# Performance work log

Measured on AMD Instinct MI355X. Metric: run time of the kernel, lower is better.

The kernel has to match this reference:

```python
import jax, jax.numpy as jnp
import numpy as np

E, W, S, Q, D = 256, 20, 5, 300, 512
ALPHA = 37.0  # hardcoded weight '37' in computeProto


def setup_inputs() -> dict:
    key = jax.random.key(0)
    k1, k2 = jax.random.split(key)
    x_shot = jax.random.normal(k1, (E, W, S, D), dtype=jnp.float32)
    x_query = jax.random.normal(k2, (E, Q, D), dtype=jnp.float32)
    temp = jnp.float32(10.0)
    return {"x_shot": x_shot, "x_query": x_query, "temp": temp}


def compute_proto(x_shot, x_query):
    # x_shot: [E, W, S, D], x_query: [E, Q, D]
    n_shot = x_shot.shape[2]
    shot_sum = x_shot.sum(axis=2)                      # [E, W, D]
    shot_mean = x_shot.mean(axis=2)                    # [E, W, D]
    # pairwise euclidean distance mean-vs-query: [E, W, Q]
    diff = shot_mean[:, :, None, :] - x_query[:, None, :, :]
    dist = jnp.sqrt(jnp.sum(diff * diff, axis=-1))
    weights = jax.nn.softmax(-dist, axis=-1)           # softmax over queries
    pooled = jnp.einsum('ewq,eqd->ewd', weights, x_query)  # [E, W, D]
    proto = (shot_sum + ALPHA * pooled) / (n_shot + ALPHA)
    return proto


def l2norm(x, axis=-1, eps=1e-12):
    n = jnp.sqrt(jnp.sum(x * x, axis=axis, keepdims=True))
    return x / jnp.maximum(n, eps)


def reference(x_shot, x_query, temp):
    proto = compute_proto(x_shot, x_query)             # [E, W, D]
    proto = l2norm(proto)
    q = l2norm(x_query)
    logits = temp * jnp.einsum('eqd,ewd->eqw', q, proto)  # [E, Q, W]
    return logits
```

## Files before the change

### kernel.cpp

```cpp
#include <hip/hip_runtime.h>
#include <math.h>

#define E_ 256
#define W_ 20
#define S_ 5
#define Q_ 300
#define D_ 512
#define ALPHA_ 37.0f
#define QCH 32
#define NCH 10
#define QPAD 304

typedef __attribute__((ext_vector_type(8))) short bf16x8;
typedef __attribute__((ext_vector_type(4))) float f32x4;
typedef __attribute__((ext_vector_type(2))) unsigned int u32x2;
typedef __attribute__((ext_vector_type(4))) unsigned int u32x4;

#define OFF_SS   0
#define OFF_XQ   20480
#define OFF_BUF  53248
#define OFF_Q2   77568
#define OFF_M2   78848
#define OFF_MINV 78976
#define OFF_RED  79104
#define LDS_BYTES 79744

__device__ __forceinline__ unsigned short f2bf(float x) {
    unsigned int u = __builtin_bit_cast(unsigned int, x);
    u += 0x7fffu + ((u >> 16) & 1u);
    return (unsigned short)(u >> 16);
}
__device__ __forceinline__ float bf2f(unsigned short h) {
    unsigned int u = ((unsigned int)h) << 16;
    return __builtin_bit_cast(float, u);
}

__device__ __forceinline__ bf16x8 ldfrag(const char* base, int row, int k0) {
    const int phys = (k0 >> 3) ^ (row & 7);
    return *reinterpret_cast<const bf16x8*>(base + row * 1024 + phys * 16);
}

__device__ __forceinline__ void stage_load(const float4* xq4, int c, int qcount,
                                           int tid, float4* r) {
    const int qr = tid >> 4;
    const int i  = tid & 15;
    const int qg = c * QCH + ((qr < qcount) ? qr : 0);
    const float4* row4 = xq4 + (size_t)qg * (D_ / 4);
    #pragma unroll
    for (int j = 0; j < 4; ++j) {
        const int ch = i + 16 * j;
        r[2 * j]     = row4[2 * ch];
        r[2 * j + 1] = row4[2 * ch + 1];
    }
}

template <bool WQ2>
__device__ __forceinline__ void stage_write(const float4* r, char* s_xq, float* s_q2,
                                            int c, int qcount, int tid) {
    const int qr = tid >> 4;
    const int i  = tid & 15;
    const bool valid = qr < qcount;
    float q2 = 0.f;
    #pragma unroll
    for (int j = 0; j < 4; ++j) {
        const int ch = i + 16 * j;
        float4 a = valid ? r[2 * j]     : make_float4(0.f, 0.f, 0.f, 0.f);
        float4 b = valid ? r[2 * j + 1] : make_float4(0.f, 0.f, 0.f, 0.f);
        if (WQ2) {
            q2 += a.x * a.x + a.y * a.y + a.z * a.z + a.w * a.w
                + b.x * b.x + b.y * b.y + b.z * b.z + b.w * b.w;
        }
        u32x4 v;
        v[0] = (unsigned int)f2bf(a.x) | ((unsigned int)f2bf(a.y) << 16);
        v[1] = (unsigned int)f2bf(a.z) | ((unsigned int)f2bf(a.w) << 16);
        v[2] = (unsigned int)f2bf(b.x) | ((unsigned int)f2bf(b.y) << 16);
        v[3] = (unsigned int)f2bf(b.z) | ((unsigned int)f2bf(b.w) << 16);
        *reinterpret_cast<u32x4*>(s_xq + qr * 1024 + ((ch ^ (qr & 7)) << 4)) = v;
    }
    if (WQ2) {
        q2 += __shfl_xor(q2, 1);
        q2 += __shfl_xor(q2, 2);
        q2 += __shfl_xor(q2, 4);
        q2 += __shfl_xor(q2, 8);
        if (i == 0) s_q2[c * QCH + qr] = valid ? q2 : 0.f;
    }
}

__global__ __launch_bounds__(512, 4) void fused9(const float* __restrict__ xs,
                                                 const float* __restrict__ xq,
                                                 const float* __restrict__ temp_p,
                                                 float* __restrict__ out) {
    extern __shared__ char smem[];
    char*  s_ss   = smem + OFF_SS;
    char*  s_xq   = smem + OFF_XQ;
    float* s_buf  = (float*)(smem + OFF_BUF);
    float* s_q2   = (float*)(smem + OFF_Q2);
    float* s_m2   = (float*)(smem + OFF_M2);
    float* s_minv = (float*)(smem + OFF_MINV);
    float* s_red  = (float*)(smem + OFF_RED);

    const int e    = blockIdx.x;
    const int tid  = threadIdx.x;
    const int lane = tid & 63;
    const int wv   = tid >> 6;
    const int ln15 = lane & 15;
    const int hi   = lane >> 4;

    const float*  xse = xs + (size_t)e * (W_ * S_ * D_);
    const float*  xqe = xq + (size_t)e * (Q_ * D_);
    const float4* xq4 = (const float4*)xqe;
    const float   temp = *temp_p;

    float4 buf[8];

    stage_load(xq4, 0, QCH, tid, buf);

    #pragma unroll
    for (int it = 0; it < 5; ++it) {
        const int idx = it * 512 + tid;
        const int w   = idx >> 7;
        const int dq  = idx & 127;
        const float4* p0 = reinterpret_cast<const float4*>(xse + (w * S_) * D_ + dq * 4);
        float4 a = p0[0];
        #pragma unroll
        for (int s = 1; s < S_; ++s) {
            const float4 t = p0[s * (D_ / 4)];
            a.x += t.x; a.y += t.y; a.z += t.z; a.w += t.w;
        }
        u32x2 v;
        v[0] = (unsigned int)f2bf(a.x) | ((unsigned int)f2bf(a.y) << 16);
        v[1] = (unsigned int)f2bf(a.z) | ((unsigned int)f2bf(a.w) << 16);
        *reinterpret_cast<u32x2*>(s_ss + w * 1024 + (((dq >> 1) ^ (w & 7)) << 4) +
                                  (dq & 1) * 8) = v;
    }
    __syncthreads();

    for (int w = wv; w < W_; w += 8) {
        bf16x8 v = *reinterpret_cast<const bf16x8*>(s_ss + w * 1024 + ((lane ^ (w & 7)) << 4));
        float p = 0.f;
        #pragma unroll
        for (int j = 0; j < 8; ++j) { float f = bf2f((unsigned short)v[j]); p += f * f; }
        #pragma unroll
        for (int off = 32; off; off >>= 1) p += __shfl_xor(p, off);
        if (lane == 0) s_m2[w] = p * (1.f / (S_ * S_));
    }
    __syncthreads();

    for (int c = 0; c < NCH; ++c) {
        const int qcount = (c == NCH - 1) ? (Q_ - (NCH - 1) * QCH) : QCH;
        stage_write<true>(buf, s_xq, s_q2, c, qcount, tid);
        __syncthreads();
        if (c + 1 < NCH)
            stage_load(xq4, c + 1, (c + 2 == NCH) ? (Q_ - (NCH - 1) * QCH) : QCH, tid, buf);

        if (wv < 4) {
            const int wtile = wv >> 1, qtile = wv & 1;
            f32x4 acc = {0.f, 0.f, 0.f, 0.f};
            const int arow = wtile * 4 + ln15;
            const int brow = qtile * 16 + ln15;
            #pragma unroll
            for (int k = 0; k < 16; ++k) {
                bf16x8 a = ldfrag(s_ss, arow, k * 32 + hi * 8);
                bf16x8 b = ldfrag(s_xq, brow, k * 32 + hi * 8);
                acc = __builtin_amdgcn_mfma_f32_16x16x32_bf16(a, b, acc, 0, 0, 0);
            }
            const int qloc = qtile * 16 + ln15;
            if (qloc < qcount) {
                const int qg = c * QCH + qloc;
                const float q2v = s_q2[qg];
                #pragma unroll
                for (int r = 0; r < 4; ++r) {
                    const int w = wtile * 4 + hi * 4 + r;
                    float d2 = s_m2[w] + q2v - 0.4f * acc[r];
                    s_buf[w * QPAD + qg] = -sqrtf(fmaxf(d2, 0.f));
                }
            }
        }
        __syncthreads();
    }

    for (int w = wv; w < W_; w += 8) {
        float mx = -1e30f;
        for (int q = lane; q < Q_; q += 64) mx = fmaxf(mx, s_buf[w * QPAD + q]);
        #pragma unroll
        for (int off = 32; off; off >>= 1) mx = fmaxf(mx, __shfl_xor(mx, off));
        float sm = 0.f;
        for (int q = lane; q < Q_; q += 64) {
            float ex = __expf(s_buf[w * QPAD + q] - mx);
            s_buf[w * QPAD + q] = ex;
            sm += ex;
        }
        #pragma unroll
        for (int off = 32; off; off >>= 1) sm += __shfl_xor(sm, off);
        const float inv = 1.f / sm;
        for (int q = lane; q < Q_; q += 64) s_buf[w * QPAD + q] *= inv;
    }
    __syncthreads();

    stage_load(xq4, 0, QCH, tid, buf);

    {
        float pr[W_];
        #pragma unroll
        for (int w = 0; w < W_; ++w) pr[w] = 0.f;
        for (int q0 = 0; q0 < Q_; q0 += 4) {
            const float qv0 = xqe[(q0 + 0) * D_ + tid];
            const float qv1 = xqe[(q0 + 1) * D_ + tid];
            const float qv2 = xqe[(q0 + 2) * D_ + tid];
            const float qv3 = xqe[(q0 + 3) * D_ + tid];
            #pragma unroll
            for (int w = 0; w < W_; ++w) {
                const float4 wt = *reinterpret_cast<const float4*>(&s_buf[w * QPAD + q0]);
                pr[w] += wt.x * qv0 + wt.y * qv1 + wt.z * qv2 + wt.w * qv3;
            }
        }
        const int chb = tid >> 3;
        #pragma unroll
        for (int w = 0; w < W_; ++w) {
            unsigned short h =
                *(unsigned short*)(s_ss + w * 1024 + ((chb ^ (w & 7)) << 4) + (tid & 7) * 2);
            pr[w] = (bf2f(h) + ALPHA_ * pr[w]) * (1.f / (S_ + ALPHA_));
        }
        #pragma unroll
        for (int w = 0; w < W_; ++w) {
            float p = pr[w] * pr[w];
            #pragma unroll
            for (int off = 32; off; off >>= 1) p += __shfl_xor(p, off);
            if (lane == 0) s_red[wv * W_ + w] = p;
        }
        __syncthreads();
        if (tid < W_) {
            float p = 0.f;
            #pragma unroll
            for (int k = 0; k < 8; ++k) p += s_red[k * W_ + tid];
            s_minv[tid] = 1.f / fmaxf(sqrtf(p), 1e-12f);
        }
        __syncthreads();
        #pragma unroll
        for (int w = 0; w < W_; ++w) {
            *(unsigned short*)(s_ss + w * 1024 + ((chb ^ (w & 7)) << 4) + (tid & 7) * 2) =
                f2bf(pr[w] * s_minv[w]);
        }
        __syncthreads();
    }

    const size_t eoff = (size_t)e * (Q_ * W_);
    for (int c = 0; c < NCH; ++c) {
        const int qcount = (c == NCH - 1) ? (Q_ - (NCH - 1) * QCH) : QCH;
        stage_write<false>(buf, s_xq, s_q2, c, qcount, tid);
        __syncthreads();
        if (c + 1 < NCH)
            stage_load(xq4, c + 1, (c + 2 == NCH) ? (Q_ - (NCH - 1) * QCH) : QCH, tid, buf);

        if (wv < 4) {
            const int qtile = wv >> 1, wtile = wv & 1;
            f32x4 acc = {0.f, 0.f, 0.f, 0.f};
            const int arow = qtile * 16 + ln15;
            const int brow = wtile * 4 + ln15;
            #pragma unroll
            for (int k = 0; k < 16; ++k) {
                bf16x8 a = ldfrag(s_xq, arow, k * 32 + hi * 8);
                bf16x8 b = ldfrag(s_ss, brow, k * 32 + hi * 8);
                acc = __builtin_amdgcn_mfma_f32_16x16x32_bf16(a, b, acc, 0, 0, 0);
            }
            const int w = wtile * 4 + ln15;
            #pragma unroll
            for (int r = 0; r < 4; ++r) {
                const int qloc = qtile * 16 + hi * 4 + r;
                if (qloc < qcount) {
                    const int qg = c * QCH + qloc;
                    const float scale = temp / fmaxf(sqrtf(s_q2[qg]), 1e-12f);
                    out[eoff + qg * W_ + w] = scale * acc[r];
                }
            }
        }
        __syncthreads();
    }
}

extern "C" void kernel_launch(void* const* d_in, const int* in_sizes, int n_in,
                              void* d_out, int out_size, void* d_ws, size_t ws_size,
                              hipStream_t stream) {
    const float* xs = (const float*)d_in[0];
    const float* xq = (const float*)d_in[1];
    const float* tp = (const float*)d_in[2];
    hipFuncSetAttribute(reinterpret_cast<const void*>(fused9),
                        hipFuncAttributeMaxDynamicSharedMemorySize, LDS_BYTES);
    fused9<<<E_, 512, LDS_BYTES, stream>>>(xs, xq, tp, (float*)d_out);
}
```

Baseline: 122.3 us.

## Widen block to 12 waves with 96-query chunks and packed bf16 conversion

Result: no change. 123.6 us (+1.1%).

```diff
diff --git a/kernel.cpp b/kernel.cpp
--- a/kernel.cpp
+++ b/kernel.cpp
@@ -1,4 +1,5 @@
 #include <hip/hip_runtime.h>
+#include <hip/hip_bf16.h>
 #include <math.h>
 
 #define E_ 256
@@ -7,8 +8,8 @@
 #define Q_ 300
 #define D_ 512
 #define ALPHA_ 37.0f
-#define QCH 32
-#define NCH 10
+#define QCH 96
+#define NCH 4
 #define QPAD 304
 
 typedef __attribute__((ext_vector_type(8))) short bf16x8;
@@ -18,17 +19,24 @@
 
 #define OFF_SS   0
 #define OFF_XQ   20480
-#define OFF_BUF  53248
-#define OFF_Q2   77568
-#define OFF_M2   78848
-#define OFF_MINV 78976
-#define OFF_RED  79104
-#define LDS_BYTES 79744
+#define OFF_BUF  118784
+#define OFF_Q2   143104
+#define OFF_M2   144640
+#define OFF_MINV 144768
+#define OFF_RED  144896
+#define LDS_BYTES 145536
 
 __device__ __forceinline__ unsigned short f2bf(float x) {
-    unsigned int u = __builtin_bit_cast(unsigned int, x);
-    u += 0x7fffu + ((u >> 16) & 1u);
-    return (unsigned short)(u >> 16);
+    __hip_bfloat16 h = __float2bfloat16(x);
+    unsigned short u;
+    __builtin_memcpy(&u, &h, 2);
+    return u;
+}
+__device__ __forceinline__ unsigned int pk2(float lo, float hi) {
+    __hip_bfloat162 h2 = __float22bfloat162_rn(make_float2(lo, hi));
+    unsigned int u;
+    __builtin_memcpy(&u, &h2, 4);
+    return u;
 }
 __device__ __forceinline__ float bf2f(unsigned short h) {
     unsigned int u = ((unsigned int)h) << 16;
@@ -42,13 +50,13 @@
 
 __device__ __forceinline__ void stage_load(const float4* xq4, int c, int qcount,
                                            int tid, float4* r) {
-    const int qr = tid >> 4;
-    const int i  = tid & 15;
+    const int qr = tid >> 3;
+    const int i  = tid & 7;
     const int qg = c * QCH + ((qr < qcount) ? qr : 0);
     const float4* row4 = xq4 + (size_t)qg * (D_ / 4);
     #pragma unroll
-    for (int j = 0; j < 4; ++j) {
-        const int ch = i + 16 * j;
+    for (int j = 0; j < 8; ++j) {
+        const int ch = i + 8 * j;
         r[2 * j]     = row4[2 * ch];
         r[2 * j + 1] = row4[2 * ch + 1];
     }
@@ -57,13 +65,13 @@
 template <bool WQ2>
 __device__ __forceinline__ void stage_write(const float4* r, char* s_xq, float* s_q2,
                                             int c, int qcount, int tid) {
-    const int qr = tid >> 4;
-    const int i  = tid & 15;
+    const int qr = tid >> 3;
+    const int i  = tid & 7;
     const bool valid = qr < qcount;
     float q2 = 0.f;
     #pragma unroll
-    for (int j = 0; j < 4; ++j) {
-        const int ch = i + 16 * j;
+    for (int j = 0; j < 8; ++j) {
+        const int ch = i + 8 * j;
         float4 a = valid ? r[2 * j]     : make_float4(0.f, 0.f, 0.f, 0.f);
         float4 b = valid ? r[2 * j + 1] : make_float4(0.f, 0.f, 0.f, 0.f);
         if (WQ2) {
@@ -71,25 +79,24 @@
                 + b.x * b.x + b.y * b.y + b.z * b.z + b.w * b.w;
         }
         u32x4 v;
-        v[0] = (unsigned int)f2bf(a.x) | ((unsigned int)f2bf(a.y) << 16);
-        v[1] = (unsigned int)f2bf(a.z) | ((unsigned int)f2bf(a.w) << 16);
-        v[2] = (unsigned int)f2bf(b.x) | ((unsigned int)f2bf(b.y) << 16);
-        v[3] = (unsigned int)f2bf(b.z) | ((unsigned int)f2bf(b.w) << 16);
+        v[0] = pk2(a.x, a.y);
+        v[1] = pk2(a.z, a.w);
+        v[2] = pk2(b.x, b.y);
+        v[3] = pk2(b.z, b.w);
         *reinterpret_cast<u32x4*>(s_xq + qr * 1024 + ((ch ^ (qr & 7)) << 4)) = v;
     }
     if (WQ2) {
         q2 += __shfl_xor(q2, 1);
         q2 += __shfl_xor(q2, 2);
         q2 += __shfl_xor(q2, 4);
-        q2 += __shfl_xor(q2, 8);
         if (i == 0) s_q2[c * QCH + qr] = valid ? q2 : 0.f;
     }
 }
 
-__global__ __launch_bounds__(512, 4) void fused9(const float* __restrict__ xs,
-                                                 const float* __restrict__ xq,
-                                                 const float* __restrict__ temp_p,
-                                                 float* __restrict__ out) {
+__global__ __launch_bounds__(768, 1) void fused13(const float* __restrict__ xs,
+                                                  const float* __restrict__ xq,
+                                                  const float* __restrict__ temp_p,
+                                                  float* __restrict__ out) {
     extern __shared__ char smem[];
     char*  s_ss   = smem + OFF_SS;
     char*  s_xq   = smem + OFF_XQ;
@@ -111,31 +118,33 @@
     const float4* xq4 = (const float4*)xqe;
     const float   temp = *temp_p;
 
-    float4 buf[8];
+    float4 buf[16];
 
     stage_load(xq4, 0, QCH, tid, buf);
 
     #pragma unroll
-    for (int it = 0; it < 5; ++it) {
-        const int idx = it * 512 + tid;
-        const int w   = idx >> 7;
-        const int dq  = idx & 127;
-        const float4* p0 = reinterpret_cast<const float4*>(xse + (w * S_) * D_ + dq * 4);
-        float4 a = p0[0];
-        #pragma unroll
-        for (int s = 1; s < S_; ++s) {
-            const float4 t = p0[s * (D_ / 4)];
-            a.x += t.x; a.y += t.y; a.z += t.z; a.w += t.w;
-        }
-        u32x2 v;
-        v[0] = (unsigned int)f2bf(a.x) | ((unsigned int)f2bf(a.y) << 16);
-        v[1] = (unsigned int)f2bf(a.z) | ((unsigned int)f2bf(a.w) << 16);
-        *reinterpret_cast<u32x2*>(s_ss + w * 1024 + (((dq >> 1) ^ (w & 7)) << 4) +
-                                  (dq & 1) * 8) = v;
+    for (int it = 0; it < 4; ++it) {
+        const int idx = it * 768 + tid;
+        if (idx < W_ * 128) {
+            const int w  = idx >> 7;
+            const int dq = idx & 127;
+            const float4* p0 = reinterpret_cast<const float4*>(xse + (w * S_) * D_ + dq * 4);
+            float4 a = p0[0];
+            #pragma unroll
+            for (int s = 1; s < S_; ++s) {
+                const float4 t = p0[s * (D_ / 4)];
+                a.x += t.x; a.y += t.y; a.z += t.z; a.w += t.w;
+            }
+            u32x2 v;
+            v[0] = pk2(a.x, a.y);
+            v[1] = pk2(a.z, a.w);
+            *reinterpret_cast<u32x2*>(s_ss + w * 1024 + (((dq >> 1) ^ (w & 7)) << 4) +
+                                      (dq & 1) * 8) = v;
+        }
     }
     __syncthreads();
 
-    for (int w = wv; w < W_; w += 8) {
+    for (int w = wv; w < W_; w += 12) {
         bf16x8 v = *reinterpret_cast<const bf16x8*>(s_ss + w * 1024 + ((lane ^ (w & 7)) << 4));
         float p = 0.f;
         #pragma unroll
@@ -153,33 +162,31 @@
         if (c + 1 < NCH)
             stage_load(xq4, c + 1, (c + 2 == NCH) ? (Q_ - (NCH - 1) * QCH) : QCH, tid, buf);
 
-        if (wv < 4) {
-            const int wtile = wv >> 1, qtile = wv & 1;
-            f32x4 acc = {0.f, 0.f, 0.f, 0.f};
-            const int arow = wtile * 4 + ln15;
-            const int brow = qtile * 16 + ln15;
-            #pragma unroll
-            for (int k = 0; k < 16; ++k) {
-                bf16x8 a = ldfrag(s_ss, arow, k * 32 + hi * 8);
-                bf16x8 b = ldfrag(s_xq, brow, k * 32 + hi * 8);
-                acc = __builtin_amdgcn_mfma_f32_16x16x32_bf16(a, b, acc, 0, 0, 0);
-            }
-            const int qloc = qtile * 16 + ln15;
-            if (qloc < qcount) {
-                const int qg = c * QCH + qloc;
-                const float q2v = s_q2[qg];
-                #pragma unroll
-                for (int r = 0; r < 4; ++r) {
-                    const int w = wtile * 4 + hi * 4 + r;
-                    float d2 = s_m2[w] + q2v - 0.4f * acc[r];
-                    s_buf[w * QPAD + qg] = -sqrtf(fmaxf(d2, 0.f));
-                }
-            }
-        }
-        __syncthreads();
-    }
-
-    for (int w = wv; w < W_; w += 8) {
+        const int qtile = wv >> 1, wtile = wv & 1;
+        f32x4 acc = {0.f, 0.f, 0.f, 0.f};
+        const int arow = wtile * 4 + ln15;
+        const int brow = qtile * 16 + ln15;
+        #pragma unroll
+        for (int k = 0; k < 16; ++k) {
+            bf16x8 a = ldfrag(s_ss, arow, k * 32 + hi * 8);
+            bf16x8 b = ldfrag(s_xq, brow, k * 32 + hi * 8);
+            acc = __builtin_amdgcn_mfma_f32_16x16x32_bf16(a, b, acc, 0, 0, 0);
+        }
+        const int qloc = qtile * 16 + ln15;
+        if (qloc < qcount) {
+            const int qg = c * QCH + qloc;
+            const float q2v = s_q2[qg];
+            #pragma unroll
+            for (int r = 0; r < 4; ++r) {
+                const int w = wtile * 4 + hi * 4 + r;
+                float d2 = s_m2[w] + q2v - 0.4f * acc[r];
+                s_buf[w * QPAD + qg] = -sqrtf(fmaxf(d2, 0.f));
+            }
+        }
+        __syncthreads();
+    }
+
+    for (int w = wv; w < W_; w += 12) {
         float mx = -1e30f;
         for (int q = lane; q < Q_; q += 64) mx = fmaxf(mx, s_buf[w * QPAD + q]);
         #pragma unroll
@@ -201,32 +208,34 @@
 
     {
         float pr[W_];
-        #pragma unroll
-        for (int w = 0; w < W_; ++w) pr[w] = 0.f;
-        for (int q0 = 0; q0 < Q_; q0 += 4) {
-            const float qv0 = xqe[(q0 + 0) * D_ + tid];
-            const float qv1 = xqe[(q0 + 1) * D_ + tid];
-            const float qv2 = xqe[(q0 + 2) * D_ + tid];
-            const float qv3 = xqe[(q0 + 3) * D_ + tid];
+        if (tid < 512) {
+            #pragma unroll
+            for (int w = 0; w < W_; ++w) pr[w] = 0.f;
+            for (int q0 = 0; q0 < Q_; q0 += 4) {
+                const float qv0 = xqe[(q0 + 0) * D_ + tid];
+                const float qv1 = xqe[(q0 + 1) * D_ + tid];
+                const float qv2 = xqe[(q0 + 2) * D_ + tid];
+                const float qv3 = xqe[(q0 + 3) * D_ + tid];
+                #pragma unroll
+                for (int w = 0; w < W_; ++w) {
+                    const float4 wt = *reinterpret_cast<const float4*>(&s_buf[w * QPAD + q0]);
+                    pr[w] += wt.x * qv0 + wt.y * qv1 + wt.z * qv2 + wt.w * qv3;
+                }
+            }
+            const int chb = tid >> 3;
             #pragma unroll
             for (int w = 0; w < W_; ++w) {
-                const float4 wt = *reinterpret_cast<const float4*>(&s_buf[w * QPAD + q0]);
-                pr[w] += wt.x * qv0 + wt.y * qv1 + wt.z * qv2 + wt.w * qv3;
-            }
-        }
-        const int chb = tid >> 3;
-        #pragma unroll
-        for (int w = 0; w < W_; ++w) {
-            unsigned short h =
-                *(unsigned short*)(s_ss + w * 1024 + ((chb ^ (w & 7)) << 4) + (tid & 7) * 2);
-            pr[w] = (bf2f(h) + ALPHA_ * pr[w]) * (1.f / (S_ + ALPHA_));
-        }
-        #pragma unroll
-        for (int w = 0; w < W_; ++w) {
-            float p = pr[w] * pr[w];
-            #pragma unroll
-            for (int off = 32; off; off >>= 1) p += __shfl_xor(p, off);
-            if (lane == 0) s_red[wv * W_ + w] = p;
+                unsigned short h =
+                    *(unsigned short*)(s_ss + w * 1024 + ((chb ^ (w & 7)) << 4) + (tid & 7) * 2);
+                pr[w] = (bf2f(h) + ALPHA_ * pr[w]) * (1.f / (S_ + ALPHA_));
+            }
+            #pragma unroll
+            for (int w = 0; w < W_; ++w) {
+                float p = pr[w] * pr[w];
+                #pragma unroll
+                for (int off = 32; off; off >>= 1) p += __shfl_xor(p, off);
+                if (lane == 0) s_red[wv * W_ + w] = p;
+            }
         }
         __syncthreads();
         if (tid < W_) {
@@ -236,10 +245,13 @@
             s_minv[tid] = 1.f / fmaxf(sqrtf(p), 1e-12f);
         }
         __syncthreads();
-        #pragma unroll
-        for (int w = 0; w < W_; ++w) {
-            *(unsigned short*)(s_ss + w * 1024 + ((chb ^ (w & 7)) << 4) + (tid & 7) * 2) =
-                f2bf(pr[w] * s_minv[w]);
+        if (tid < 512) {
+            const int chb = tid >> 3;
+            #pragma unroll
+            for (int w = 0; w < W_; ++w) {
+                *(unsigned short*)(s_ss + w * 1024 + ((chb ^ (w & 7)) << 4) + (tid & 7) * 2) =
+                    f2bf(pr[w] * s_minv[w]);
+            }
         }
         __syncthreads();
     }
@@ -252,26 +264,24 @@
         if (c + 1 < NCH)
             stage_load(xq4, c + 1, (c + 2 == NCH) ? (Q_ - (NCH - 1) * QCH) : QCH, tid, buf);
 
-        if (wv < 4) {
-            const int qtile = wv >> 1, wtile = wv & 1;
-            f32x4 acc = {0.f, 0.f, 0.f, 0.f};
-            const int arow = qtile * 16 + ln15;
-            const int brow = wtile * 4 + ln15;
-            #pragma unroll
-            for (int k = 0; k < 16; ++k) {
-                bf16x8 a = ldfrag(s_xq, arow, k * 32 + hi * 8);
-                bf16x8 b = ldfrag(s_ss, brow, k * 32 + hi * 8);
-                acc = __builtin_amdgcn_mfma_f32_16x16x32_bf16(a, b, acc, 0, 0, 0);
-            }
-            const int w = wtile * 4 + ln15;
-            #pragma unroll
-            for (int r = 0; r < 4; ++r) {
-                const int qloc = qtile * 16 + hi * 4 + r;
-                if (qloc < qcount) {
-                    const int qg = c * QCH + qloc;
-                    const float scale = temp / fmaxf(sqrtf(s_q2[qg]), 1e-12f);
-                    out[eoff + qg * W_ + w] = scale * acc[r];
-                }
+        const int qtile = wv >> 1, wtile = wv & 1;
+        f32x4 acc = {0.f, 0.f, 0.f, 0.f};
+        const int arow = qtile * 16 + ln15;
+        const int brow = wtile * 4 + ln15;
+        #pragma unroll
+        for (int k = 0; k < 16; ++k) {
+            bf16x8 a = ldfrag(s_xq, arow, k * 32 + hi * 8);
+            bf16x8 b = ldfrag(s_ss, brow, k * 32 + hi * 8);
+            acc = __builtin_amdgcn_mfma_f32_16x16x32_bf16(a, b, acc, 0, 0, 0);
+        }
+        const int w = wtile * 4 + ln15;
+        #pragma unroll
+        for (int r = 0; r < 4; ++r) {
+            const int qloc = qtile * 16 + hi * 4 + r;
+            if (qloc < qcount) {
+                const int qg = c * QCH + qloc;
+                const float scale = temp / fmaxf(sqrtf(s_q2[qg]), 1e-12f);
+                out[eoff + qg * W_ + w] = scale * acc[r];
             }
         }
         __syncthreads();
@@ -284,7 +294,7 @@
     const float* xs = (const float*)d_in[0];
     const float* xq = (const float*)d_in[1];
     const float* tp = (const float*)d_in[2];
-    hipFuncSetAttribute(reinterpret_cast<const void*>(fused9),
-                        hipFuncAttributeMaxDynamicSharedMemorySize, LDS_BYTES);
-    fused9<<<E_, 512, LDS_BYTES, stream>>>(xs, xq, tp, (float*)d_out);
-}
+    (void)hipFuncSetAttribute(reinterpret_cast<const void*>(fused13),
+                              hipFuncAttributeMaxDynamicSharedMemorySize, LDS_BYTES);
+    fused13<<<E_, 768, LDS_BYTES, stream>>>(xs, xq, tp, (float*)d_out);
+}
```
